# Kernel optimization log

Hardware: AMD Instinct MI355X
Metric: run time of the kernel (lower is better)

Reference implementation:

```python
import jax, jax.numpy as jnp
import numpy as np

N0, N1, N2 = 512, 2048, 8192   # targets, hop1, hop2 node counts
K = 33                          # nneighbor + self loop
IN, HID, OUT, NH = 256, 128, 128, 8
NEG = -9.0e15
ALPHA = 0.2                     # LeakyReLU negative slope


def setup_inputs() -> dict:
    key = jax.random.key(0)
    ks = jax.random.split(key, 8)
    feats = jax.random.normal(ks[0], (N2, IN), jnp.float32)
    # xavier-ish scaled params (gain 1.414)
    W1 = jax.random.normal(ks[1], (NH, IN, HID), jnp.float32) * 0.072
    a1 = jax.random.normal(ks[2], (NH, 2 * HID), jnp.float32) * 0.105
    W2 = jax.random.normal(ks[3], (HID * NH, OUT), jnp.float32) * 0.042
    a2 = jax.random.normal(ks[4], (2 * OUT,), jnp.float32) * 0.105
    # layer1 edges: each of N1 targets gets K distinct neighbors in [0, N2)
    tgt1 = jnp.repeat(jnp.arange(N1, dtype=jnp.int32), K)
    dst1 = ((jnp.arange(N1)[:, None] * 97 + jnp.arange(K)[None, :] * 131) % N2).astype(jnp.int32).reshape(-1)
    src1 = jax.random.randint(ks[5], (N1 * K,), 0, N2, jnp.int32)
    # layer2 edges: each of N0 targets gets K distinct neighbors in [0, N1)
    tgt2 = jnp.repeat(jnp.arange(N0, dtype=jnp.int32), K)
    dst2 = ((jnp.arange(N0)[:, None] * 53 + jnp.arange(K)[None, :] * 61) % N1).astype(jnp.int32).reshape(-1)
    src2 = jax.random.randint(ks[6], (N0 * K,), 0, N1, jnp.int32)
    return dict(feats=feats, W1=W1, a1=a1, W2=W2, a2=a2,
                src1=src1, dst1=dst1, tgt1=tgt1, src2=src2, dst2=dst2, tgt2=tgt2)


def gat_layer(x, W, a, src, dst, tgt, t_len):
    # x: [n, in], W: [in, d], a: [2d]
    h = x @ W                                   # [n, d]
    d = h.shape[1]
    # concat([h[src], h[dst]]) @ a  ==  h[src]@a[:d] + h[dst]@a[d:]
    e = h[src] @ a[:d] + h[dst] @ a[d:]         # [E]
    e = jnp.where(e > 0, e, ALPHA * e)          # LeakyReLU
    att = jnp.full((t_len, h.shape[0]), NEG, h.dtype).at[tgt, dst].set(e)
    att = jax.nn.softmax(att, axis=1)           # dense row softmax (masked entries ~0)
    return jax.nn.elu(att @ h)                  # [t_len, d]


def reference(feats, W1, a1, W2, a2, src1, dst1, tgt1, src2, dst2, tgt2):
    # layer 1: nhead independent GAT heads over hop2 features
    heads = jax.vmap(lambda W, a: gat_layer(feats, W, a, src1, dst1, tgt1, N1))(W1, a1)  # [NH, N1, HID]
    x = jnp.transpose(heads, (1, 0, 2)).reshape(N1, NH * HID)  # torch.cat(dim=1)
    # layer 2: single GAT layer producing [N0, OUT]
    return gat_layer(x, W2, a2, src2, dst2, tgt2, N0)
```

## Files before the change

### kernel.cpp

```cpp
#include <hip/hip_runtime.h>
#include <math.h>

#define ALPHA 0.2f

constexpr int CN0 = 512, CN1 = 2048, CN2 = 8192, CK = 33;
constexpr int CIN = 256, CHID = 128, CNH = 8;

using u16    = unsigned short;
using f32x4  = __attribute__((ext_vector_type(4))) float;
using bf16x8 = __attribute__((ext_vector_type(8))) short;
using short8 = __attribute__((ext_vector_type(8))) short;

__device__ __forceinline__ u16 f2bf(float f) {
    unsigned u = __float_as_uint(f);
    u += 0x7fff + ((u >> 16) & 1);
    return (u16)(u >> 16);
}
__device__ __forceinline__ float bf2f(u16 h) {
    return __uint_as_float(((unsigned)h) << 16);
}

#define GLD16(g, l)                                                        \
    __builtin_amdgcn_global_load_lds(                                      \
        (const __attribute__((address_space(1))) void*)(g),                \
        (__attribute__((address_space(3))) void*)(l), 16, 0, 0)

__global__ __launch_bounds__(256) void prep_k(const float* __restrict__ feats,
                                              u16* __restrict__ fb,
                                              const float* __restrict__ W1,
                                              u16* __restrict__ w1t,
                                              const float* __restrict__ W2,
                                              u16* __restrict__ w2t) {
    __shared__ float t[32][33];
    int b = blockIdx.x;
    if (b < 2048) {
        const int i = (b * 256 + threadIdx.x) * 4;
        const float4 v = *reinterpret_cast<const float4*>(feats + i);
        *reinterpret_cast<ushort4*>(fb + i) =
            make_ushort4(f2bf(v.x), f2bf(v.y), f2bf(v.z), f2bf(v.w));
        return;
    }
    b -= 2048;
    const float* ip;
    u16* op;
    int R, C, r0, c0;
    if (b < 256) {
        const int h = b >> 5, w = b & 31;
        ip = W1 + (size_t)h * CIN * CHID;
        op = w1t + (size_t)h * CIN * CHID;
        R = CIN; C = CHID; r0 = (w >> 2) * 32; c0 = (w & 3) * 32;
    } else {
        b -= 256;
        ip = W2; op = w2t;
        R = CNH * CHID; C = CHID; r0 = (b >> 2) * 32; c0 = (b & 3) * 32;
    }
    const int tx = threadIdx.x & 31, ty = threadIdx.x >> 5;
#pragma unroll
    for (int i = 0; i < 4; ++i)
        t[ty + 8 * i][tx] = ip[(size_t)(r0 + ty + 8 * i) * C + c0 + tx];
    __syncthreads();
#pragma unroll
    for (int i = 0; i < 4; ++i)
        op[(size_t)(c0 + ty + 8 * i) * R + r0 + tx] = f2bf(t[tx][ty + 8 * i]);
}

template <int KSTEPS, bool BF16OUT, bool SCORES>
__global__ __launch_bounds__(256) void gemm_mfma(const u16* __restrict__ A, int lda,
                                                 const u16* __restrict__ Bt, int ldb,
                                                 u16* __restrict__ Cb,
                                                 float* __restrict__ Cf, int ldc,
                                                 long csplit,
                                                 const float* __restrict__ av,
                                                 float* __restrict__ s1o,
                                                 float* __restrict__ s2o,
                                                 int snodes) {
    __shared__ __attribute__((aligned(16))) u16 As[128 * 32];
    __shared__ __attribute__((aligned(16))) u16 Bs[128 * 32];

    const int tid  = threadIdx.x;
    const int lane = tid & 63;
    const int wave = tid >> 6;
    const int row0 = blockIdx.x * 128;
    const int col0 = blockIdx.y * 128;
    const int kbase = blockIdx.z * (KSTEPS * 32);
    const int wr = (wave >> 1) * 64;
    const int wc = (wave & 1) * 64;

    f32x4 acc[4][4];
#pragma unroll
    for (int m = 0; m < 4; ++m)
#pragma unroll
        for (int n = 0; n < 4; ++n) acc[m][n] = (f32x4){0.f, 0.f, 0.f, 0.f};

    const int r0c = tid >> 2;
    const int cs0 = tid & 3;
    const int c0  = (cs0 - (r0c >> 1)) & 3;
    const int r1c = r0c + 64;

    const u16* ga0 = A + (size_t)(row0 + r0c) * lda + kbase + c0 * 8;
    const u16* ga1 = A + (size_t)(row0 + r1c) * lda + kbase + c0 * 8;
    const u16* gb0 = Bt + (size_t)(col0 + r0c) * ldb + kbase + c0 * 8;
    const u16* gb1 = Bt + (size_t)(col0 + r1c) * ldb + kbase + c0 * 8;
    u16* As0 = As + wave * 512;
    u16* As1 = As + 2048 + wave * 512;
    u16* Bs0 = Bs + wave * 512;
    u16* Bs1 = Bs + 2048 + wave * 512;

    for (int s = 0; s < KSTEPS; ++s) {
        const int k0 = s * 32;
        GLD16(ga0 + k0, As0);
        GLD16(ga1 + k0, As1);
        GLD16(gb0 + k0, Bs0);
        GLD16(gb1 + k0, Bs1);
        __syncthreads();

        bf16x8 af[4], bfr[4];
#pragma unroll
        for (int m = 0; m < 4; ++m) {
            const int rt = wr + m * 16 + (lane & 15);
            const int cs = ((lane >> 4) + (rt >> 1)) & 3;
            af[m] = *reinterpret_cast<const bf16x8*>(&As[rt * 32 + cs * 8]);
            const int rt2 = wc + m * 16 + (lane & 15);
            const int cs2 = ((lane >> 4) + (rt2 >> 1)) & 3;
            bfr[m] = *reinterpret_cast<const bf16x8*>(&Bs[rt2 * 32 + cs2 * 8]);
        }
#pragma unroll
        for (int m = 0; m < 4; ++m)
#pragma unroll
            for (int n = 0; n < 4; ++n)
                acc[m][n] = __builtin_amdgcn_mfma_f32_16x16x32_bf16(
                    af[m], bfr[n], acc[m][n], 0, 0, 0);
        __syncthreads();
    }

    if constexpr (BF16OUT) {
        __shared__ __attribute__((aligned(16))) u16 Cs[128 * 136];
#pragma unroll
        for (int m = 0; m < 4; ++m) {
            const int rr = wr + m * 16 + (lane >> 4) * 4;
#pragma unroll
            for (int n = 0; n < 4; ++n) {
                const int cc = wc + n * 16 + (lane & 15);
#pragma unroll
                for (int q = 0; q < 4; ++q)
                    Cs[(rr + q) * 136 + cc] = f2bf(acc[m][n][q]);
            }
        }
        __syncthreads();
#pragma unroll
        for (int i = 0; i < 8; ++i) {
            const int cid = i * 256 + tid;
            const int r  = cid >> 4;
            const int kc = cid & 15;
            const int4 v = *reinterpret_cast<const int4*>(&Cs[r * 136 + kc * 8]);
            *reinterpret_cast<int4*>(&Cb[(long)(row0 + r) * ldc + col0 + kc * 8]) = v;
        }
    } else {
        const long cbase = (long)blockIdx.z * csplit;
#pragma unroll
        for (int m = 0; m < 4; ++m) {
            const int rr = row0 + wr + m * 16 + (lane >> 4) * 4;
#pragma unroll
            for (int n = 0; n < 4; ++n) {
                const int cc = col0 + wc + n * 16 + (lane & 15);
#pragma unroll
                for (int q = 0; q < 4; ++q)
                    Cf[cbase + (long)(rr + q) * ldc + cc] = acc[m][n][q];
            }
        }
    }

    if constexpr (SCORES) {
        __shared__ float sred1[2][128];
        __shared__ float sred2[2][128];
        const int head = blockIdx.y;
        float av1[4], av2[4];
#pragma unroll
        for (int n = 0; n < 4; ++n) {
            const int c = wc + n * 16 + (lane & 15);
            av1[n] = av[head * 2 * CHID + c];
            av2[n] = av[head * 2 * CHID + CHID + c];
        }
        float p1[4][4], p2[4][4];
#pragma unroll
        for (int m = 0; m < 4; ++m)
#pragma unroll
            for (int q = 0; q < 4; ++q) {
                float t1 = 0.f, t2 = 0.f;
#pragma unroll
                for (int n = 0; n < 4; ++n) {
                    t1 = fmaf(acc[m][n][q], av1[n], t1);
                    t2 = fmaf(acc[m][n][q], av2[n], t2);
                }
#pragma unroll
                for (int mk = 1; mk < 16; mk <<= 1) {
                    t1 += __shfl_xor(t1, mk);
                    t2 += __shfl_xor(t2, mk);
                }
                p1[m][q] = t1;
                p2[m][q] = t2;
            }
        if ((lane & 15) == 0) {
            const int g = lane >> 4;
#pragma unroll
            for (int m = 0; m < 4; ++m)
#pragma unroll
                for (int q = 0; q < 4; ++q) {
                    sred1[wave & 1][wr + m * 16 + g * 4 + q] = p1[m][q];
                    sred2[wave & 1][wr + m * 16 + g * 4 + q] = p2[m][q];
                }
        }
        __syncthreads();
        if (tid < 128) {
            s1o[head * snodes + row0 + tid] = sred1[0][tid] + sred1[1][tid];
            s2o[head * snodes + row0 + tid] = sred2[0][tid] + sred2[1][tid];
        }
    }
}

__global__ __launch_bounds__(128) void agg1_k(const float* __restrict__ s1,
                                              const float* __restrict__ s2,
                                              const int* __restrict__ src,
                                              const int* __restrict__ dst,
                                              const u16* __restrict__ hm,
                                              u16* __restrict__ xout) {
    __shared__ float wgt[CNH][CK];
    __shared__ int dsts[CK];

    const int t    = blockIdx.x;
    const int tid  = threadIdx.x;
    const int wv   = tid >> 6;
    const int lane = tid & 63;

    int sv = 0, dv = 0;
    if (lane < CK) {
        sv = src[t * CK + lane];
        dv = dst[t * CK + lane];
        if (tid < CK) dsts[tid] = dv;
    }
#pragma unroll
    for (int hh = 0; hh < 4; ++hh) {
        const int head = wv * 4 + hh;
        float e = -3.0e38f;
        if (lane < CK) {
            const float ee = s1[head * CN2 + sv] + s2[head * CN2 + dv];
            e = (ee > 0.f) ? ee : ALPHA * ee;
        }
        float m = e;
#pragma unroll
        for (int mm = 1; mm < 64; mm <<= 1) m = fmaxf(m, __shfl_xor(m, mm));
        const float p = (lane < CK) ? __expf(e - m) : 0.f;
        float s = p;
#pragma unroll
        for (int mm = 1; mm < 64; mm <<= 1) s += __shfl_xor(s, mm);
        if (lane < CK) wgt[head][lane] = p / s;
    }
    __syncthreads();

    const int c0   = tid * 8;
    const int head = tid >> 4;
    float acc[8] = {0.f, 0.f, 0.f, 0.f, 0.f, 0.f, 0.f, 0.f};
#pragma unroll
    for (int k = 0; k < CK; ++k) {
        const short8 hv = *reinterpret_cast<const short8*>(
            hm + (size_t)dsts[k] * (CNH * CHID) + c0);
        const float w = wgt[head][k];
#pragma unroll
        for (int j = 0; j < 8; ++j) acc[j] = fmaf(w, bf2f((u16)hv[j]), acc[j]);
    }
    short8 o;
#pragma unroll
    for (int j = 0; j < 8; ++j) {
        const float v = (acc[j] > 0.f) ? acc[j] : __expf(acc[j]) - 1.f;
        o[j] = (short)f2bf(v);
    }
    *reinterpret_cast<short8*>(xout + (size_t)t * (CNH * CHID) + c0) = o;
}

__global__ __launch_bounds__(256) void scores2_k(const float* __restrict__ part,
                                                 const float* __restrict__ a,
                                                 float* __restrict__ h2,
                                                 float* __restrict__ s1,
                                                 float* __restrict__ s2) {
    const int wid  = (blockIdx.x * 256 + threadIdx.x) >> 6;
    const int lane = threadIdx.x & 63;
    const int j = lane * 2;
    float x0 = 0.f, x1 = 0.f;
#pragma unroll
    for (int sp = 0; sp < 8; ++sp) {
        const float2 v = *reinterpret_cast<const float2*>(
            part + (size_t)sp * CN1 * CHID + (size_t)wid * CHID + j);
        x0 += v.x; x1 += v.y;
    }
    *reinterpret_cast<float2*>(h2 + (size_t)wid * CHID + j) = make_float2(x0, x1);
    float d1 = x0 * a[j] + x1 * a[j + 1];
    float d2 = x0 * a[CHID + j] + x1 * a[CHID + j + 1];
#pragma unroll
    for (int m = 1; m < 64; m <<= 1) {
        d1 += __shfl_xor(d1, m);
        d2 += __shfl_xor(d2, m);
    }
    if (lane == 0) { s1[wid] = d1; s2[wid] = d2; }
}

__global__ __launch_bounds__(256) void agg2_k(const float* __restrict__ s1,
                                              const float* __restrict__ s2,
                                              const int* __restrict__ src,
                                              const int* __restrict__ dst,
                                              const float* __restrict__ h2,
                                              float* __restrict__ out) {
    const int t    = (blockIdx.x * 256 + threadIdx.x) >> 6;
    const int lane = threadIdx.x & 63;

    float e = -3.0e38f;
    int dv = 0;
    if (lane < CK) {
        const int sv = src[t * CK + lane];
        dv = dst[t * CK + lane];
        const float ee = s1[sv] + s2[dv];
        e = (ee > 0.f) ? ee : ALPHA * ee;
    }
    float m = e;
#pragma unroll
    for (int mm = 1; mm < 64; mm <<= 1) m = fmaxf(m, __shfl_xor(m, mm));
    float p = (lane < CK) ? __expf(e - m) : 0.f;
    float ssum = p;
#pragma unroll
    for (int mm = 1; mm < 64; mm <<= 1) ssum += __shfl_xor(ssum, mm);
    const float invs = 1.f / ssum;

    float a0 = 0.f, a1 = 0.f;
#pragma unroll
    for (int k = 0; k < CK; ++k) {
        const float w = __shfl(p, k) * invs;
        const int d = __shfl(dv, k);
        const float2 hv = *reinterpret_cast<const float2*>(h2 + (size_t)d * CHID + lane * 2);
        a0 = fmaf(w, hv.x, a0);
        a1 = fmaf(w, hv.y, a1);
    }
    a0 = (a0 > 0.f) ? a0 : __expf(a0) - 1.f;
    a1 = (a1 > 0.f) ? a1 : __expf(a1) - 1.f;
    *reinterpret_cast<float2*>(out + (size_t)t * CHID + lane * 2) = make_float2(a0, a1);
}

extern "C" void kernel_launch(void* const* d_in, const int* in_sizes, int n_in,
                              void* d_out, int out_size, void* d_ws, size_t ws_size,
                              hipStream_t stream) {
    const float* feats = (const float*)d_in[0];
    const float* W1    = (const float*)d_in[1];
    const float* a1    = (const float*)d_in[2];
    const float* W2    = (const float*)d_in[3];
    const float* a2    = (const float*)d_in[4];
    const int*   src1  = (const int*)d_in[5];
    const int*   dst1  = (const int*)d_in[6];
    const int*   src2  = (const int*)d_in[8];
    const int*   dst2  = (const int*)d_in[9];
    float* out = (float*)d_out;

    char* w = (char*)d_ws;
    u16*   fb   = (u16*)w;                 w += (size_t)CN2 * CIN * 2;
    u16*   w1t  = (u16*)w;                 w += (size_t)CNH * CIN * CHID * 2;
    u16*   w2t  = (u16*)w;                 w += (size_t)CNH * CHID * CHID * 2;
    u16*   h1b  = (u16*)w;                 w += (size_t)CN2 * CNH * CHID * 2;
    float* s1   = (float*)w;               w += (size_t)CNH * CN2 * 4;
    float* s2   = (float*)w;               w += (size_t)CNH * CN2 * 4;
    u16*   xb   = (u16*)w;                 w += (size_t)CN1 * CNH * CHID * 2;
    float* part = (float*)w;               w += (size_t)8 * CN1 * CHID * 4;
    float* h2   = (float*)w;               w += (size_t)CN1 * CHID * 4;
    float* s21  = (float*)w;               w += (size_t)CN1 * 4;
    float* s22  = (float*)w;               w += (size_t)CN1 * 4;

    prep_k<<<dim3(2048 + 256 + 128), 256, 0, stream>>>(feats, fb, W1, w1t, W2, w2t);

    gemm_mfma<8, true, true><<<dim3(CN2 / 128, (CNH * CHID) / 128), 256, 0, stream>>>(
        fb, CIN, w1t, CIN, h1b, nullptr, CNH * CHID, 0, a1, s1, s2, CN2);

    agg1_k<<<dim3(CN1), 128, 0, stream>>>(s1, s2, src1, dst1, h1b, xb);

    gemm_mfma<4, false, false><<<dim3(CN1 / 128, 1, 8), 256, 0, stream>>>(
        xb, CNH * CHID, w2t, CNH * CHID, nullptr, part, CHID, (long)CN1 * CHID,
        nullptr, nullptr, nullptr, 0);

    scores2_k<<<dim3(CN1 / 4), 256, 0, stream>>>(part, a2, h2, s21, s22);

    agg2_k<<<dim3(CN0 / 4), 256, 0, stream>>>(s21, s22, src2, dst2, h2, out);
}
```

Before: 60.19 us.

## Double-buffer GEMM LDS tiles to overlap global loads with MFMA

Converts the MFMA GEMM to a two-stage LDS ping-pong: the next K-step's global-to-LDS loads are issued before computing the current step, so one barrier per iteration remains. LDS is unified into one buffer that is reused for the bf16 output staging tile. This aims to hide global load latency behind matrix-core work, at the cost of doubled LDS for staging, which may lower occupancy. Correctness depends on the async LDS loads being complete before the barrier, and the code adds no explicit vmcnt wait.

```diff
diff --git a/kernel.cpp b/kernel.cpp
--- a/kernel.cpp
+++ b/kernel.cpp
@@ -74,8 +74,8 @@
                                                  float* __restrict__ s1o,
                                                  float* __restrict__ s2o,
                                                  int snodes) {
-    __shared__ __attribute__((aligned(16))) u16 As[128 * 32];
-    __shared__ __attribute__((aligned(16))) u16 Bs[128 * 32];
+    constexpr int SMEMSZ = BF16OUT ? (128 * 136 * 2) : 32768;
+    __shared__ __attribute__((aligned(16))) char smem[SMEMSZ];
 
     const int tid  = threadIdx.x;
     const int lane = tid & 63;
@@ -101,28 +101,36 @@
     const u16* ga1 = A + (size_t)(row0 + r1c) * lda + kbase + c0 * 8;
     const u16* gb0 = Bt + (size_t)(col0 + r0c) * ldb + kbase + c0 * 8;
     const u16* gb1 = Bt + (size_t)(col0 + r1c) * ldb + kbase + c0 * 8;
-    u16* As0 = As + wave * 512;
-    u16* As1 = As + 2048 + wave * 512;
-    u16* Bs0 = Bs + wave * 512;
-    u16* Bs1 = Bs + 2048 + wave * 512;
+
+    auto STAGE = [&](int s) {
+        const int k0 = s * 32;
+        char* base = smem + (s & 1) * 16384;
+        u16* as = (u16*)base + wave * 512;
+        u16* bs = (u16*)(base + 8192) + wave * 512;
+        GLD16(ga0 + k0, as);
+        GLD16(ga1 + k0, as + 2048);
+        GLD16(gb0 + k0, bs);
+        GLD16(gb1 + k0, bs + 2048);
+    };
+
+    STAGE(0);
+    __syncthreads();
 
     for (int s = 0; s < KSTEPS; ++s) {
-        const int k0 = s * 32;
-        GLD16(ga0 + k0, As0);
-        GLD16(ga1 + k0, As1);
-        GLD16(gb0 + k0, Bs0);
-        GLD16(gb1 + k0, Bs1);
-        __syncthreads();
+        if (s + 1 < KSTEPS) STAGE(s + 1);
+
+        const u16* Acur = (const u16*)(smem + (s & 1) * 16384);
+        const u16* Bcur = Acur + 4096;
 
         bf16x8 af[4], bfr[4];
 #pragma unroll
         for (int m = 0; m < 4; ++m) {
             const int rt = wr + m * 16 + (lane & 15);
             const int cs = ((lane >> 4) + (rt >> 1)) & 3;
-            af[m] = *reinterpret_cast<const bf16x8*>(&As[rt * 32 + cs * 8]);
+            af[m] = *reinterpret_cast<const bf16x8*>(Acur + rt * 32 + cs * 8);
             const int rt2 = wc + m * 16 + (lane & 15);
             const int cs2 = ((lane >> 4) + (rt2 >> 1)) & 3;
-            bfr[m] = *reinterpret_cast<const bf16x8*>(&Bs[rt2 * 32 + cs2 * 8]);
+            bfr[m] = *reinterpret_cast<const bf16x8*>(Bcur + rt2 * 32 + cs2 * 8);
         }
 #pragma unroll
         for (int m = 0; m < 4; ++m)
@@ -130,11 +138,12 @@
             for (int n = 0; n < 4; ++n)
                 acc[m][n] = __builtin_amdgcn_mfma_f32_16x16x32_bf16(
                     af[m], bfr[n], acc[m][n], 0, 0, 0);
+
         __syncthreads();
     }
 
     if constexpr (BF16OUT) {
-        __shared__ __attribute__((aligned(16))) u16 Cs[128 * 136];
+        u16* Cs = (u16*)smem;
 #pragma unroll
         for (int m = 0; m < 4; ++m) {
             const int rr = wr + m * 16 + (lane >> 4) * 4;
```

Result: no change. 60.02 us (-0.3%).
